# Performance work log

Hardware: AMD Instinct MI355X
Metric: run time of the kernel (lower is better)

The kernel has to match this reference:

```python
import jax, jax.numpy as jnp
import numpy as np

B, T, C, NH, HS, NL, VOCAB = 4, 1024, 768, 12, 64, 6, 128
PRIMES = [2, 3, 5, 7, 11, 13, 17, 19, 23, 29]
NEG_INF = jnp.finfo(jnp.float32).min


def _build_lut(t):
    # lut[n, i] = v_{p_i}(n), p-adic valuation of position n
    lut = np.zeros((t + 1, len(PRIMES)), np.float32)
    for pi, p in enumerate(PRIMES):
        nn = np.arange(t + 1, dtype=np.int64)
        nn[0] = 1  # v_p(0) treated as 0
        while (nn % p == 0).any():
            d = nn % p == 0
            lut[d, pi] += 1.0
            nn[d] //= p
    return lut


def _build_buffers(t):
    lut = _build_lut(t)
    vl = lut[1 : t + 1]  # positions 1..T, [T, 10]
    res = np.minimum(vl[:, None, :], vl[None, :, :]).sum(-1)  # [T, T]
    causal = np.tril(np.ones((t, t), dtype=bool))
    allowed = ((res > 0) | np.eye(t, dtype=bool)) & causal
    rbias = (np.log1p(res) * allowed).astype(np.float32)
    return vl.astype(np.float32), rbias, allowed


def setup_inputs() -> dict:
    key = jax.random.key(0)
    ks = jax.random.split(key, 16)
    s = 0.02
    vl, rbias, allowed = _build_buffers(T)
    return {
        "idx": jax.random.randint(ks[0], (B, T), 0, VOCAB, dtype=jnp.int32),
        "tok_emb": jax.random.normal(ks[1], (VOCAB, C)) * s,
        "pe_w": jax.random.normal(ks[2], (10, C)) * s,
        "pe_b": jnp.zeros((C,)),
        "vlut": jnp.asarray(vl),
        "rbias": jnp.asarray(rbias),
        "allowed": jnp.asarray(allowed),
        "ln1_g": jnp.ones((NL, C)),
        "ln1_b": jnp.zeros((NL, C)),
        "qw": jax.random.normal(ks[3], (NL, NH, C, HS)) * s,
        "kw": jax.random.normal(ks[4], (NL, NH, C, HS)) * s,
        "vw": jax.random.normal(ks[5], (NL, NH, C, HS)) * s,
        "proj_w": jax.random.normal(ks[6], (NL, C, C)) * s,
        "proj_b": jnp.zeros((NL, C)),
        "ln2_g": jnp.ones((NL, C)),
        "ln2_b": jnp.zeros((NL, C)),
        "ff1_w": jax.random.normal(ks[7], (NL, C, 4 * C)) * s,
        "ff1_b": jnp.zeros((NL, 4 * C)),
        "ff2_w": jax.random.normal(ks[8], (NL, 4 * C, C)) * s,
        "ff2_b": jnp.zeros((NL, C)),
        "lnf_g": jnp.ones((C,)),
        "lnf_b": jnp.zeros((C,)),
        "head_w": jax.random.normal(ks[9], (C, VOCAB)) * s,
        "head_b": jnp.zeros((VOCAB,)),
    }


def _ln(x, g, b, eps=1e-5):
    m = x.mean(-1, keepdims=True)
    v = ((x - m) ** 2).mean(-1, keepdims=True)
    return (x - m) * jax.lax.rsqrt(v + eps) * g + b


def reference(idx, tok_emb, pe_w, pe_b, vlut, rbias, allowed,
              ln1_g, ln1_b, qw, kw, vw, proj_w, proj_b,
              ln2_g, ln2_b, ff1_w, ff1_b, ff2_w, ff2_b,
              lnf_g, lnf_b, head_w, head_b):
    # token embedding + spectral positional encoding
    x = tok_emb[idx] + (vlut @ pe_w + pe_b)  # [B, T, C]
    scale = C ** (-0.5)  # NOTE: source scales by full embed dim, not head_size
    for l in range(NL):
        h = _ln(x, ln1_g[l], ln1_b[l])
        q = jnp.einsum("btc,hcd->bhtd", h, qw[l])
        k = jnp.einsum("btc,hcd->bhtd", h, kw[l])
        v = jnp.einsum("btc,hcd->bhtd", h, vw[l])
        w = jnp.einsum("bhtd,bhsd->bhts", q, k) * scale + rbias  # [B,H,T,T]
        w = jnp.where(allowed, w, NEG_INF)
        a = jax.nn.softmax(w, axis=-1)
        o = jnp.einsum("bhts,bhsd->bhtd", a, v)
        o = o.transpose(0, 2, 1, 3).reshape(x.shape[0], x.shape[1], C)
        x = x + o @ proj_w[l] + proj_b[l]
        h2 = _ln(x, ln2_g[l], ln2_b[l])
        x = x + jax.nn.gelu(h2 @ ff1_w[l] + ff1_b[l], approximate=False) @ ff2_w[l] + ff2_b[l]
    return _ln(x, lnf_g, lnf_b) @ head_w + head_b  # [B, T, VOCAB]
```

## Files before the change

kernel.cpp:

```cpp
#include <hip/hip_runtime.h>
#include <hip/hip_bf16.h>
#include <math.h>


#define Bz 4
#define Tz 1024
#define Cz 768
#define NHz 12
#define HSz 64
#define NLz 6
#define VOCABz 128
#define NTOK (Bz * Tz)

typedef __hip_bfloat16 bf16;
typedef __attribute__((ext_vector_type(8))) __bf16 bf16x8;
typedef __attribute__((ext_vector_type(4))) float f32x4;

#define MFMA16(a, b, c) __builtin_amdgcn_mfma_f32_16x16x32_bf16(a, b, c, 0, 0, 0)

__device__ __forceinline__ float bf2f(bf16 x) { return __bfloat162float(x); }
__device__ __forceinline__ bf16 f2bf(float x) { return __float2bfloat16(x); }
__device__ __forceinline__ float ldx(const void* p, size_t i, int f) {
  return f ? bf2f(((const bf16*)p)[i]) : ((const float*)p)[i];
}
__device__ __forceinline__ void async16(const bf16* g, bf16* l) {
  __builtin_amdgcn_global_load_lds(
      (const __attribute__((address_space(1))) unsigned int*)g,
      (__attribute__((address_space(3))) unsigned int*)l, 16, 0, 0);
}

__global__ void detect_kernel(const void* g1, int* flag) {
  if (threadIdx.x == 0) {
    const unsigned short* p = (const unsigned short*)g1;
    int cnt = 0;
    for (int i = 0; i < 64; i++) cnt += (p[i] == 0x3F80u) ? 1 : 0;
    *flag = (cnt >= 60) ? 1 : 0;
  }
}

#define NCONV 15
struct CPack {
  const void* s[NCONV];
  bf16* d[NCONV];
  int n[NCONV];
};
__global__ __launch_bounds__(256) void convert_all(CPack p, const int* __restrict__ flagp) {
  int f = *flagp;
  int stride = gridDim.x * 256;
#pragma unroll 1
  for (int t = 0; t < NCONV; t++) {
    int n = p.n[t];
    const void* src = p.s[t];
    bf16* dst = p.d[t];
    for (int i = blockIdx.x * 256 + threadIdx.x; i < n; i += stride)
      dst[i] = f ? ((const bf16*)src)[i] : f2bf(((const float*)src)[i]);
  }
}

__global__ __launch_bounds__(256) void transpose_tiled(
    const void* __restrict__ src, bf16* __restrict__ dst, int R, int C,
    size_t s_mat, size_t d_base, size_t d_l, size_t d_h, int hmod,
    const int* __restrict__ flagp) {
  __shared__ bf16 t[64][65];
  int f = *flagp;
  int c0 = blockIdx.x * 64, r0 = blockIdx.y * 64;
  int z = blockIdx.z;
  size_t so = (size_t)z * s_mat;
  size_t dofs = d_base + (size_t)(z / hmod) * d_l + (size_t)(z % hmod) * d_h;
  int tr = threadIdx.x >> 2;
  int tc = (threadIdx.x & 3) * 16;
  size_t sbase = so + (size_t)(r0 + tr) * C + c0 + tc;
#pragma unroll
  for (int u = 0; u < 16; u++) t[tr][tc + u] = f2bf(ldx(src, sbase + u, f));
  __syncthreads();
  int wc = threadIdx.x >> 2;
  int wr = (threadIdx.x & 3) * 16;
  bf16* dp = dst + dofs + (size_t)(c0 + wc) * R + r0 + wr;
#pragma unroll
  for (int u = 0; u < 16; u++) dp[u] = t[wr + u][wc];
}

__global__ __launch_bounds__(256) void embed_kernel(
    const int* __restrict__ idx, const bf16* __restrict__ tok_emb,
    const bf16* __restrict__ pe_w, const bf16* __restrict__ pe_b,
    const bf16* __restrict__ vlut, float* __restrict__ x_res) {
  int row = blockIdx.x;
  int t = row % Tz;
  int tok = idx[row];
  float vl[10];
#pragma unroll
  for (int p = 0; p < 10; p++) vl[p] = bf2f(vlut[t * 10 + p]);
  for (int c = threadIdx.x; c < Cz; c += 256) {
    float acc = bf2f(tok_emb[(size_t)tok * Cz + c]) + bf2f(pe_b[c]);
#pragma unroll
    for (int p = 0; p < 10; p++) acc += vl[p] * bf2f(pe_w[p * Cz + c]);
    x_res[(size_t)row * Cz + c] = acc;
  }
}

__global__ __launch_bounds__(256) void ln_kernel(
    const float* __restrict__ x, const bf16* __restrict__ g,
    const bf16* __restrict__ b, bf16* __restrict__ out) {
  __shared__ float r1[4], r2[4];
  int row = blockIdx.x, tid = threadIdx.x;
  const float* xr = x + (size_t)row * Cz;
  float v0 = xr[tid], v1 = xr[tid + 256], v2 = xr[tid + 512];
  float s1 = v0 + v1 + v2, s2 = v0 * v0 + v1 * v1 + v2 * v2;
#pragma unroll
  for (int off = 32; off > 0; off >>= 1) {
    s1 += __shfl_down(s1, off);
    s2 += __shfl_down(s2, off);
  }
  int lane = tid & 63, wid = tid >> 6;
  if (lane == 0) { r1[wid] = s1; r2[wid] = s2; }
  __syncthreads();
  s1 = r1[0] + r1[1] + r1[2] + r1[3];
  s2 = r2[0] + r2[1] + r2[2] + r2[3];
  float m = s1 * (1.0f / Cz);
  float var = s2 * (1.0f / Cz) - m * m;
  float inv = rsqrtf(var + 1e-5f);
  bf16* orow = out + (size_t)row * Cz;
  orow[tid] = f2bf((v0 - m) * inv * bf2f(g[tid]) + bf2f(b[tid]));
  orow[tid + 256] = f2bf((v1 - m) * inv * bf2f(g[tid + 256]) + bf2f(b[tid + 256]));
  orow[tid + 512] = f2bf((v2 - m) * inv * bf2f(g[tid + 512]) + bf2f(b[tid + 512]));
}

template <int MT>
__global__ __launch_bounds__(256) void gemm_mfma(
    const bf16* __restrict__ A, const bf16* __restrict__ Wt,
    const bf16* __restrict__ bias, float* __restrict__ resid,
    void* __restrict__ out, int M, int N, int K, int mode,
    const int* __restrict__ flagp) {
  constexpr int TM = MT * 32;
  constexpr int API = MT / 2;
  __shared__ bf16 ldsA[2][TM * 32];
  __shared__ bf16 ldsB[2][4096];
  int tid = threadIdx.x;
  int lane = tid & 63, w = tid >> 6;
  int wm = (w >> 1) * (MT * 16), wn = (w & 1) * 64;
  int q = lane >> 4, ln = lane & 15;
  int m0 = blockIdx.y * TM, n0 = blockIdx.x * 128;

  const bf16* gA[API];
  const bf16* gB[2];
#pragma unroll
  for (int p = 0; p < API; p++) {
    int o = w * (API * 1024) + p * 1024 + lane * 16;
    int rp = o >> 7, pp = (o >> 4) & 7;
    int pl = pp ^ (rp & 7);
    int row = rp * 2 + (pl >> 2);
    int cb = pl & 3;
    gA[p] = A + (size_t)(m0 + row) * K + cb * 8;
  }
#pragma unroll
  for (int p = 0; p < 2; p++) {
    int o = w * 2048 + p * 1024 + lane * 16;
    int rp = o >> 7, pp = (o >> 4) & 7;
    int pl = pp ^ (rp & 7);
    int row = rp * 2 + (pl >> 2);
    int cb = pl & 3;
    gB[p] = Wt + (size_t)(n0 + row) * K + cb * 8;
  }
  int ppf = (((ln & 1) << 2) | q) ^ (ln >> 1);
  int aoff = wm * 32 + (ln >> 1) * 64 + ppf * 8;
  int boff = wn * 32 + (ln >> 1) * 64 + ppf * 8;

  f32x4 acc[MT][4] = {};
#pragma unroll
  for (int p = 0; p < API; p++)
    async16(gA[p], &ldsA[0][w * (API * 512) + p * 512]);
#pragma unroll
  for (int p = 0; p < 2; p++)
    async16(gB[p], &ldsB[0][w * 1024 + p * 512]);
  int cur = 0;
  for (int k0 = 0; k0 < K; k0 += 32) {
    __syncthreads();
    if (k0 + 32 < K) {
      int nxt = cur ^ 1;
#pragma unroll
      for (int p = 0; p < API; p++)
        async16(gA[p] + k0 + 32, &ldsA[nxt][w * (API * 512) + p * 512]);
#pragma unroll
      for (int p = 0; p < 2; p++)
        async16(gB[p] + k0 + 32, &ldsB[nxt][w * 1024 + p * 512]);
    }
    bf16x8 af[MT], bfr[4];
#pragma unroll
    for (int i = 0; i < MT; i++)
      af[i] = *(const bf16x8*)&ldsA[cur][aoff + i * 512];
#pragma unroll
    for (int j = 0; j < 4; j++)
      bfr[j] = *(const bf16x8*)&ldsB[cur][boff + j * 512];
#pragma unroll
    for (int i = 0; i < MT; i++)
#pragma unroll
      for (int j = 0; j < 4; j++)
        acc[i][j] = MFMA16(af[i], bfr[j], acc[i][j]);
    cur ^= 1;
  }
  int f = *flagp;
  float bj[4];
#pragma unroll
  for (int j = 0; j < 4; j++)
    bj[j] = bias ? bf2f(bias[n0 + wn + j * 16 + ln]) : 0.0f;
#pragma unroll
  for (int i = 0; i < MT; i++) {
#pragma unroll
    for (int j = 0; j < 4; j++) {
      int col = n0 + wn + j * 16 + ln;
#pragma unroll
      for (int r = 0; r < 4; r++) {
        int row = m0 + wm + i * 16 + q * 4 + r;
        float v = acc[i][j][r] + bj[j];
        size_t oi = (size_t)row * N + col;
        if (mode == 0) {
          ((bf16*)out)[oi] = f2bf(v);
        } else if (mode == 1) {
          ((bf16*)out)[oi] = f2bf(v * 0.5f * (1.0f + erff(v * 0.70710678118f)));
        } else if (mode == 2) {
          resid[oi] += v;
        } else {
          if (f) ((bf16*)out)[oi] = f2bf(v);
          else ((float*)out)[oi] = v;
        }
      }
    }
  }
}

#define ATS 72
__global__ __launch_bounds__(256) void transpose_v(
    const bf16* __restrict__ qkv, bf16* __restrict__ Vt) {
  __shared__ bf16 tile[64][ATS];
  int tid = threadIdx.x;
  int s0 = blockIdx.x * 64, bh = blockIdx.y;
  int b = bh / NHz, h = bh % NHz;
  int row = tid >> 2, c0 = (tid & 3) * 16;
  const bf16* src = qkv + ((size_t)(b * Tz + s0 + row)) * (3 * Cz) + 2 * Cz + h * HSz + c0;
  *(uint4*)&tile[row][c0] = *(const uint4*)src;
  *(uint4*)&tile[row][c0 + 8] = *(const uint4*)(src + 8);
  __syncthreads();
  int d = tid >> 2, sc0 = (tid & 3) * 16;
  unsigned int u[8];
#pragma unroll
  for (int m = 0; m < 8; m++) {
    unsigned int lo = *(const unsigned short*)&tile[sc0 + 2 * m][d];
    unsigned int hi = *(const unsigned short*)&tile[sc0 + 2 * m + 1][d];
    u[m] = lo | (hi << 16);
  }
  bf16* dst = Vt + ((size_t)bh * HSz + d) * Tz + s0 + sc0;
  ((uint4*)dst)[0] = make_uint4(u[0], u[1], u[2], u[3]);
  ((uint4*)dst)[1] = make_uint4(u[4], u[5], u[6], u[7]);
}

__global__ __launch_bounds__(256) void attn_flash(
    const bf16* __restrict__ qkv, const bf16* __restrict__ Vt,
    const bf16* __restrict__ rbias, bf16* __restrict__ attn_out) {
  __shared__ bf16 Qs[128][ATS];
  __shared__ bf16 Ks[64][ATS];
  __shared__ bf16 Vs[64][ATS];
  __shared__ bf16 Ps[4][32][ATS];
  int tid = threadIdx.x;
  int lane = tid & 63, w = tid >> 6;
  int q = lane >> 4, ln = lane & 15;
  int qt = 7 - blockIdx.x;
  int t0 = qt * 128, bh = blockIdx.y;
  int b = bh / NHz, h = bh % NHz;
  const float scale = 0.03608439182435161f;
  int srow = tid >> 2, sc = (tid & 3) * 16;
#pragma unroll
  for (int pass = 0; pass < 2; pass++) {
    int r = srow + pass * 64;
    const bf16* src = qkv + ((size_t)(b * Tz + t0 + r)) * (3 * Cz) + h * HSz + sc;
    *(uint4*)&Qs[r][sc] = *(const uint4*)src;
    *(uint4*)&Qs[r][sc + 8] = *(const uint4*)(src + 8);
  }
  float mrow[2][4], lrow[2][4];
  f32x4 Oacc[2][4] = {};
#pragma unroll
  for (int i = 0; i < 2; i++)
#pragma unroll
    for (int r = 0; r < 4; r++) { mrow[i][r] = -3.0e38f; lrow[i][r] = 0.0f; }
  int nk = 2 * qt + 2;

  for (int kt = 0; kt < nk; kt++) {
    int s0 = kt * 64;
    __syncthreads();
    {
      const bf16* ksrc = qkv + ((size_t)(b * Tz + s0 + srow)) * (3 * Cz) + Cz + h * HSz + sc;
      *(uint4*)&Ks[srow][sc] = *(const uint4*)ksrc;
      *(uint4*)&Ks[srow][sc + 8] = *(const uint4*)(ksrc + 8);
      const bf16* vsrc = Vt + ((size_t)bh * HSz + srow) * Tz + s0 + sc;
      *(uint4*)&Vs[srow][sc] = *(const uint4*)vsrc;
      *(uint4*)&Vs[srow][sc + 8] = *(const uint4*)(vsrc + 8);
    }
    __syncthreads();
    f32x4 sacc[2][4] = {};
#pragma unroll
    for (int ks = 0; ks < 64; ks += 32) {
      bf16x8 aq[2];
#pragma unroll
      for (int i = 0; i < 2; i++)
        aq[i] = *(const bf16x8*)&Qs[w * 32 + i * 16 + ln][ks + q * 8];
#pragma unroll
      for (int j = 0; j < 4; j++) {
        bf16x8 bk = *(const bf16x8*)&Ks[j * 16 + ln][ks + q * 8];
#pragma unroll
        for (int i = 0; i < 2; i++) sacc[i][j] = MFMA16(aq[i], bk, sacc[i][j]);
      }
    }
    float sval[2][4][4];
#pragma unroll
    for (int i = 0; i < 2; i++) {
#pragma unroll
      for (int j = 0; j < 4; j++) {
        int s_col = s0 + j * 16 + ln;
#pragma unroll
        for (int r = 0; r < 4; r++) {
          int t_row = t0 + w * 32 + i * 16 + q * 4 + r;
          float rb = bf2f(rbias[(size_t)t_row * Tz + s_col]);
          float v = sacc[i][j][r] * scale + rb;
          bool ok = (s_col <= t_row) && ((rb > 0.0f) || (s_col == t_row));
          sval[i][j][r] = ok ? v : -3.0e38f;
        }
      }
    }
    float pf[2][4][4];
#pragma unroll
    for (int i = 0; i < 2; i++) {
      float rmax[4], psum[4];
#pragma unroll
      for (int r = 0; r < 4; r++)
        rmax[r] = fmaxf(fmaxf(sval[i][0][r], sval[i][1][r]),
                        fmaxf(sval[i][2][r], sval[i][3][r]));
#pragma unroll
      for (int msk = 8; msk >= 1; msk >>= 1)
#pragma unroll
        for (int r = 0; r < 4; r++)
          rmax[r] = fmaxf(rmax[r], __shfl_xor(rmax[r], msk));
      float nme[4], alpha[4];
#pragma unroll
      for (int r = 0; r < 4; r++) {
        float nm = fmaxf(mrow[i][r], rmax[r]);
        nme[r] = (nm < -1.0e37f) ? 0.0f : nm;
        alpha[r] = (mrow[i][r] < -1.0e37f) ? 0.0f : __expf(mrow[i][r] - nm);
        mrow[i][r] = nm;
        psum[r] = 0.0f;
      }
#pragma unroll
      for (int j = 0; j < 4; j++)
#pragma unroll
        for (int r = 0; r < 4; r++) {
          float p = __expf(sval[i][j][r] - nme[r]);
          pf[i][j][r] = p;
          psum[r] += p;
        }
#pragma unroll
      for (int msk = 8; msk >= 1; msk >>= 1)
#pragma unroll
        for (int r = 0; r < 4; r++) psum[r] += __shfl_xor(psum[r], msk);
#pragma unroll
      for (int r = 0; r < 4; r++) lrow[i][r] = alpha[r] * lrow[i][r] + psum[r];
#pragma unroll
      for (int jd = 0; jd < 4; jd++)
#pragma unroll
        for (int r = 0; r < 4; r++) Oacc[i][jd][r] *= alpha[r];
#pragma unroll
      for (int j = 0; j < 4; j++)
#pragma unroll
        for (int r = 0; r < 4; r++)
          Ps[w][i * 16 + q * 4 + r][j * 16 + ln] = f2bf(pf[i][j][r]);
    }
#pragma unroll
    for (int ks = 0; ks < 64; ks += 32) {
      bf16x8 pa[2];
#pragma unroll
      for (int i = 0; i < 2; i++)
        pa[i] = *(const bf16x8*)&Ps[w][i * 16 + ln][ks + q * 8];
#pragma unroll
      for (int jd = 0; jd < 4; jd++) {
        bf16x8 vb = *(const bf16x8*)&Vs[jd * 16 + ln][ks + q * 8];
#pragma unroll
        for (int i = 0; i < 2; i++) Oacc[i][jd] = MFMA16(pa[i], vb, Oacc[i][jd]);
      }
    }
  }
#pragma unroll
  for (int i = 0; i < 2; i++)
#pragma unroll
    for (int r = 0; r < 4; r++) {
      float inv = 1.0f / lrow[i][r];
      int t_row = t0 + w * 32 + i * 16 + q * 4 + r;
#pragma unroll
      for (int jd = 0; jd < 4; jd++) {
        attn_out[(size_t)(b * Tz + t_row) * Cz + h * HSz + jd * 16 + ln] =
            f2bf(Oacc[i][jd][r] * inv);
      }
    }
}

extern "C" void kernel_launch(void* const* d_in, const int* in_sizes, int n_in,
                              void* d_out, int out_size, void* d_ws, size_t ws_size,
                              hipStream_t stream) {
  const int* idx = (const int*)d_in[0];
  int p0 = 7;
  if (n_in == 23) p0 = 6;
  else if (in_sizes[6] != Tz * Tz) p0 = 6;

  const void* r_tok_emb = d_in[1];
  const void* r_pe_w = d_in[2];
  const void* r_pe_b = d_in[3];
  const void* r_vlut = d_in[4];
  const void* r_rbias = d_in[5];
  const void* r_ln1_g = d_in[p0 + 0];
  const void* r_ln1_b = d_in[p0 + 1];
  const void* r_qw = d_in[p0 + 2];
  const void* r_kw = d_in[p0 + 3];
  const void* r_vw = d_in[p0 + 4];
  const void* r_proj_w = d_in[p0 + 5];
  const void* r_proj_b = d_in[p0 + 6];
  const void* r_ln2_g = d_in[p0 + 7];
  const void* r_ln2_b = d_in[p0 + 8];
  const void* r_ff1_w = d_in[p0 + 9];
  const void* r_ff1_b = d_in[p0 + 10];
  const void* r_ff2_w = d_in[p0 + 11];
  const void* r_ff2_b = d_in[p0 + 12];
  const void* r_lnf_g = d_in[p0 + 13];
  const void* r_lnf_b = d_in[p0 + 14];
  const void* r_head_w = d_in[p0 + 15];
  const void* r_head_b = d_in[p0 + 16];

  char* wsp = (char*)d_ws;
  auto alloc = [&](size_t bytes) {
    char* p = wsp;
    wsp += (bytes + 255) & ~(size_t)255;
    return (void*)p;
  };
  int* flag = (int*)alloc(256);
  float* x_res = (float*)alloc((size_t)NTOK * Cz * 4);
  bf16* h = (bf16*)alloc((size_t)NTOK * Cz * 2);
  bf16* qkv = (bf16*)alloc((size_t)NTOK * 3 * Cz * 2);
  bf16* attn = (bf16*)alloc((size_t)NTOK * Cz * 2);
  bf16* ffm = (bf16*)alloc((size_t)NTOK * 4 * Cz * 2);
  bf16* Vt = (bf16*)alloc((size_t)Bz * NHz * HSz * Tz * 2);
  bf16* wqkv_t = (bf16*)alloc((size_t)NLz * 3 * Cz * Cz * 2);
  bf16* proj_t = (bf16*)alloc((size_t)NLz * Cz * Cz * 2);
  bf16* ff1_t = (bf16*)alloc((size_t)NLz * 4 * Cz * Cz * 2);
  bf16* ff2_t = (bf16*)alloc((size_t)NLz * 4 * Cz * Cz * 2);
  bf16* head_t = (bf16*)alloc((size_t)VOCABz * Cz * 2);
  bf16* tok_emb = (bf16*)alloc((size_t)VOCABz * Cz * 2);
  bf16* pe_w = (bf16*)alloc(10 * Cz * 2);
  bf16* pe_b = (bf16*)alloc(Cz * 2);
  bf16* vlut = (bf16*)alloc(Tz * 10 * 2);
  bf16* rbias = (bf16*)alloc((size_t)Tz * Tz * 2);
  bf16* ln1_g = (bf16*)alloc(NLz * Cz * 2);
  bf16* ln1_b = (bf16*)alloc(NLz * Cz * 2);
  bf16* proj_b = (bf16*)alloc(NLz * Cz * 2);
  bf16* ln2_g = (bf16*)alloc(NLz * Cz * 2);
  bf16* ln2_b = (bf16*)alloc(NLz * Cz * 2);
  bf16* ff1_b = (bf16*)alloc(NLz * 4 * Cz * 2);
  bf16* ff2_b = (bf16*)alloc(NLz * Cz * 2);
  bf16* lnf_g = (bf16*)alloc(Cz * 2);
  bf16* lnf_b = (bf16*)alloc(Cz * 2);
  bf16* head_b = (bf16*)alloc(VOCABz * 2);

  detect_kernel<<<1, 64, 0, stream>>>(r_ln1_g, flag);

  CPack cp;
  const void* csrc[NCONV] = {r_tok_emb, r_pe_w, r_pe_b, r_vlut, r_rbias,
                             r_ln1_g, r_ln1_b, r_proj_b, r_ln2_g, r_ln2_b,
                             r_ff1_b, r_ff2_b, r_lnf_g, r_lnf_b, r_head_b};
  bf16* cdst[NCONV] = {tok_emb, pe_w, pe_b, vlut, rbias,
                       ln1_g, ln1_b, proj_b, ln2_g, ln2_b,
                       ff1_b, ff2_b, lnf_g, lnf_b, head_b};
  int cn[NCONV] = {VOCABz * Cz, 10 * Cz, Cz, Tz * 10, Tz * Tz,
                   NLz * Cz, NLz * Cz, NLz * Cz, NLz * Cz, NLz * Cz,
                   NLz * 4 * Cz, NLz * Cz, Cz, Cz, VOCABz};
  for (int i = 0; i < NCONV; i++) { cp.s[i] = csrc[i]; cp.d[i] = cdst[i]; cp.n[i] = cn[i]; }
  convert_all<<<1024, 256, 0, stream>>>(cp, flag);

  for (int g = 0; g < 3; g++) {
    const void* src = (g == 0) ? r_qw : (g == 1) ? r_kw : r_vw;
    transpose_tiled<<<dim3(1, Cz / 64, NLz * NHz), 256, 0, stream>>>(
        src, wqkv_t, Cz, HSz, (size_t)Cz * HSz,
        (size_t)g * Cz * Cz, (size_t)3 * Cz * Cz, (size_t)HSz * Cz, NHz, flag);
  }
  transpose_tiled<<<dim3(Cz / 64, Cz / 64, NLz), 256, 0, stream>>>(
      r_proj_w, proj_t, Cz, Cz, (size_t)Cz * Cz, 0, (size_t)Cz * Cz, 0, 1, flag);
  transpose_tiled<<<dim3(4 * Cz / 64, Cz / 64, NLz), 256, 0, stream>>>(
      r_ff1_w, ff1_t, Cz, 4 * Cz, (size_t)4 * Cz * Cz, 0, (size_t)4 * Cz * Cz, 0, 1, flag);
  transpose_tiled<<<dim3(Cz / 64, 4 * Cz / 64, NLz), 256, 0, stream>>>(
      r_ff2_w, ff2_t, 4 * Cz, Cz, (size_t)4 * Cz * Cz, 0, (size_t)4 * Cz * Cz, 0, 1, flag);
  transpose_tiled<<<dim3(VOCABz / 64, Cz / 64, 1), 256, 0, stream>>>(
      r_head_w, head_t, Cz, VOCABz, 0, 0, 0, 0, 1, flag);

  embed_kernel<<<NTOK, 256, 0, stream>>>(idx, tok_emb, pe_w, pe_b, vlut, x_res);

  for (int l = 0; l < NLz; l++) {
    ln_kernel<<<NTOK, 256, 0, stream>>>(x_res, ln1_g + l * Cz, ln1_b + l * Cz, h);
    gemm_mfma<4><<<dim3(3 * Cz / 128, NTOK / 128), 256, 0, stream>>>(
        h, wqkv_t + (size_t)l * 3 * Cz * Cz, nullptr, nullptr, qkv,
        NTOK, 3 * Cz, Cz, 0, flag);
    transpose_v<<<dim3(Tz / 64, Bz * NHz), 256, 0, stream>>>(qkv, Vt);
    attn_flash<<<dim3(Tz / 128, Bz * NHz), 256, 0, stream>>>(qkv, Vt, rbias, attn);
    gemm_mfma<2><<<dim3(Cz / 128, NTOK / 64), 256, 0, stream>>>(
        attn, proj_t + (size_t)l * Cz * Cz, proj_b + l * Cz, x_res, nullptr,
        NTOK, Cz, Cz, 2, flag);
    ln_kernel<<<NTOK, 256, 0, stream>>>(x_res, ln2_g + l * Cz, ln2_b + l * Cz, h);
    gemm_mfma<4><<<dim3(4 * Cz / 128, NTOK / 128), 256, 0, stream>>>(
        h, ff1_t + (size_t)l * 4 * Cz * Cz, ff1_b + (size_t)l * 4 * Cz, nullptr,
        ffm, NTOK, 4 * Cz, Cz, 1, flag);
    gemm_mfma<2><<<dim3(Cz / 128, NTOK / 64), 256, 0, stream>>>(
        ffm, ff2_t + (size_t)l * 4 * Cz * Cz, ff2_b + l * Cz, x_res, nullptr,
        NTOK, Cz, 4 * Cz, 2, flag);
  }
  ln_kernel<<<NTOK, 256, 0, stream>>>(x_res, lnf_g, lnf_b, h);
  gemm_mfma<2><<<dim3(VOCABz / 128, NTOK / 64), 256, 0, stream>>>(
      h, head_t, head_b, nullptr, d_out, NTOK, VOCABz, Cz, 3, flag);
}
```

Before: 2.116 ms.

## Use one wave per LayerNorm row and smaller attention query tiles with K/V prefetch

LayerNorm now assigns one wavefront per row, so a block handles four rows and the reduction uses only shuffles, with no shared memory or block barrier. The flash-attention kernel shrinks its query tile from 128 to 64 rows, which doubles the grid to give more blocks and less causal waste per block. It also prefetches the next K/V tile into registers while the current tile is being computed. In exchange, each K/V tile is loaded twice as often across blocks and each wave has less MFMA work to hide latency behind.

```diff
diff --git a/kernel.cpp b/kernel.cpp
--- a/kernel.cpp
+++ b/kernel.cpp
@@ -101,28 +101,31 @@
 __global__ __launch_bounds__(256) void ln_kernel(
     const float* __restrict__ x, const bf16* __restrict__ g,
     const bf16* __restrict__ b, bf16* __restrict__ out) {
-  __shared__ float r1[4], r2[4];
-  int row = blockIdx.x, tid = threadIdx.x;
+  int w = threadIdx.x >> 6, lane = threadIdx.x & 63;
+  int row = blockIdx.x * 4 + w;
   const float* xr = x + (size_t)row * Cz;
-  float v0 = xr[tid], v1 = xr[tid + 256], v2 = xr[tid + 512];
-  float s1 = v0 + v1 + v2, s2 = v0 * v0 + v1 * v1 + v2 * v2;
-#pragma unroll
-  for (int off = 32; off > 0; off >>= 1) {
-    s1 += __shfl_down(s1, off);
-    s2 += __shfl_down(s2, off);
-  }
-  int lane = tid & 63, wid = tid >> 6;
-  if (lane == 0) { r1[wid] = s1; r2[wid] = s2; }
-  __syncthreads();
-  s1 = r1[0] + r1[1] + r1[2] + r1[3];
-  s2 = r2[0] + r2[1] + r2[2] + r2[3];
+  float v[12];
+  float s1 = 0.0f, s2 = 0.0f;
+#pragma unroll
+  for (int i = 0; i < 12; i++) {
+    v[i] = xr[lane + i * 64];
+    s1 += v[i];
+    s2 += v[i] * v[i];
+  }
+#pragma unroll
+  for (int off = 32; off >= 1; off >>= 1) {
+    s1 += __shfl_xor(s1, off);
+    s2 += __shfl_xor(s2, off);
+  }
   float m = s1 * (1.0f / Cz);
   float var = s2 * (1.0f / Cz) - m * m;
   float inv = rsqrtf(var + 1e-5f);
   bf16* orow = out + (size_t)row * Cz;
-  orow[tid] = f2bf((v0 - m) * inv * bf2f(g[tid]) + bf2f(b[tid]));
-  orow[tid + 256] = f2bf((v1 - m) * inv * bf2f(g[tid + 256]) + bf2f(b[tid + 256]));
-  orow[tid + 512] = f2bf((v2 - m) * inv * bf2f(g[tid + 512]) + bf2f(b[tid + 512]));
+#pragma unroll
+  for (int i = 0; i < 12; i++) {
+    int c = lane + i * 64;
+    orow[c] = f2bf((v[i] - m) * inv * bf2f(g[c]) + bf2f(b[c]));
+  }
 }
 
 template <int MT>
@@ -256,147 +259,141 @@
 __global__ __launch_bounds__(256) void attn_flash(
     const bf16* __restrict__ qkv, const bf16* __restrict__ Vt,
     const bf16* __restrict__ rbias, bf16* __restrict__ attn_out) {
-  __shared__ bf16 Qs[128][ATS];
+  __shared__ bf16 Qs[64][ATS];
   __shared__ bf16 Ks[64][ATS];
   __shared__ bf16 Vs[64][ATS];
-  __shared__ bf16 Ps[4][32][ATS];
+  __shared__ bf16 Ps[4][16][ATS];
   int tid = threadIdx.x;
   int lane = tid & 63, w = tid >> 6;
   int q = lane >> 4, ln = lane & 15;
-  int qt = 7 - blockIdx.x;
-  int t0 = qt * 128, bh = blockIdx.y;
+  int qt = (int)gridDim.x - 1 - (int)blockIdx.x;
+  int t0 = qt * 64, bh = blockIdx.y;
   int b = bh / NHz, h = bh % NHz;
   const float scale = 0.03608439182435161f;
   int srow = tid >> 2, sc = (tid & 3) * 16;
-#pragma unroll
-  for (int pass = 0; pass < 2; pass++) {
-    int r = srow + pass * 64;
-    const bf16* src = qkv + ((size_t)(b * Tz + t0 + r)) * (3 * Cz) + h * HSz + sc;
-    *(uint4*)&Qs[r][sc] = *(const uint4*)src;
-    *(uint4*)&Qs[r][sc + 8] = *(const uint4*)(src + 8);
-  }
-  float mrow[2][4], lrow[2][4];
-  f32x4 Oacc[2][4] = {};
-#pragma unroll
-  for (int i = 0; i < 2; i++)
-#pragma unroll
-    for (int r = 0; r < 4; r++) { mrow[i][r] = -3.0e38f; lrow[i][r] = 0.0f; }
-  int nk = 2 * qt + 2;
-
+  {
+    const bf16* src = qkv + ((size_t)(b * Tz + t0 + srow)) * (3 * Cz) + h * HSz + sc;
+    *(uint4*)&Qs[srow][sc] = *(const uint4*)src;
+    *(uint4*)&Qs[srow][sc + 8] = *(const uint4*)(src + 8);
+  }
+  float mrow[4], lrow[4];
+  f32x4 Oacc[4] = {};
+#pragma unroll
+  for (int r = 0; r < 4; r++) { mrow[r] = -3.0e38f; lrow[r] = 0.0f; }
+  int t_base = t0 + w * 16 + q * 4;
+  int nk = qt + 1;
+
+  const bf16* kcol = qkv + (size_t)b * Tz * (3 * Cz) + Cz + h * HSz + sc;
+  const bf16* vrow = Vt + ((size_t)bh * HSz + srow) * Tz + sc;
+  uint4 ka, kb, va, vb2;
+  {
+    const bf16* kp = kcol + (size_t)srow * (3 * Cz);
+    ka = *(const uint4*)kp;
+    kb = *(const uint4*)(kp + 8);
+    va = *(const uint4*)vrow;
+    vb2 = *(const uint4*)(vrow + 8);
+  }
   for (int kt = 0; kt < nk; kt++) {
+    __syncthreads();
+    *(uint4*)&Ks[srow][sc] = ka;
+    *(uint4*)&Ks[srow][sc + 8] = kb;
+    *(uint4*)&Vs[srow][sc] = va;
+    *(uint4*)&Vs[srow][sc + 8] = vb2;
+    __syncthreads();
+    if (kt + 1 < nk) {
+      const bf16* kp = kcol + (size_t)(((kt + 1) * 64) + srow) * (3 * Cz);
+      ka = *(const uint4*)kp;
+      kb = *(const uint4*)(kp + 8);
+      const bf16* vp = vrow + (kt + 1) * 64;
+      va = *(const uint4*)vp;
+      vb2 = *(const uint4*)(vp + 8);
+    }
     int s0 = kt * 64;
-    __syncthreads();
-    {
-      const bf16* ksrc = qkv + ((size_t)(b * Tz + s0 + srow)) * (3 * Cz) + Cz + h * HSz + sc;
-      *(uint4*)&Ks[srow][sc] = *(const uint4*)ksrc;
-      *(uint4*)&Ks[srow][sc + 8] = *(const uint4*)(ksrc + 8);
-      const bf16* vsrc = Vt + ((size_t)bh * HSz + srow) * Tz + s0 + sc;
-      *(uint4*)&Vs[srow][sc] = *(const uint4*)vsrc;
-      *(uint4*)&Vs[srow][sc + 8] = *(const uint4*)(vsrc + 8);
-    }
-    __syncthreads();
-    f32x4 sacc[2][4] = {};
+    f32x4 sacc[4] = {};
 #pragma unroll
     for (int ks = 0; ks < 64; ks += 32) {
-      bf16x8 aq[2];
-#pragma unroll
-      for (int i = 0; i < 2; i++)
-        aq[i] = *(const bf16x8*)&Qs[w * 32 + i * 16 + ln][ks + q * 8];
+      bf16x8 aq = *(const bf16x8*)&Qs[w * 16 + ln][ks + q * 8];
 #pragma unroll
       for (int j = 0; j < 4; j++) {
         bf16x8 bk = *(const bf16x8*)&Ks[j * 16 + ln][ks + q * 8];
-#pragma unroll
-        for (int i = 0; i < 2; i++) sacc[i][j] = MFMA16(aq[i], bk, sacc[i][j]);
+        sacc[j] = MFMA16(aq, bk, sacc[j]);
       }
     }
-    float sval[2][4][4];
-#pragma unroll
-    for (int i = 0; i < 2; i++) {
-#pragma unroll
-      for (int j = 0; j < 4; j++) {
-        int s_col = s0 + j * 16 + ln;
-#pragma unroll
-        for (int r = 0; r < 4; r++) {
-          int t_row = t0 + w * 32 + i * 16 + q * 4 + r;
-          float rb = bf2f(rbias[(size_t)t_row * Tz + s_col]);
-          float v = sacc[i][j][r] * scale + rb;
-          bool ok = (s_col <= t_row) && ((rb > 0.0f) || (s_col == t_row));
-          sval[i][j][r] = ok ? v : -3.0e38f;
-        }
+    float sval[4][4];
+#pragma unroll
+    for (int j = 0; j < 4; j++) {
+      int s_col = s0 + j * 16 + ln;
+#pragma unroll
+      for (int r = 0; r < 4; r++) {
+        int t_row = t_base + r;
+        float rb = bf2f(rbias[(size_t)t_row * Tz + s_col]);
+        float v = sacc[j][r] * scale + rb;
+        bool ok = (s_col <= t_row) && ((rb > 0.0f) || (s_col == t_row));
+        sval[j][r] = ok ? v : -3.0e38f;
       }
     }
-    float pf[2][4][4];
-#pragma unroll
-    for (int i = 0; i < 2; i++) {
-      float rmax[4], psum[4];
+    float rmax[4];
+#pragma unroll
+    for (int r = 0; r < 4; r++)
+      rmax[r] = fmaxf(fmaxf(sval[0][r], sval[1][r]), fmaxf(sval[2][r], sval[3][r]));
+#pragma unroll
+    for (int msk = 8; msk >= 1; msk >>= 1)
 #pragma unroll
       for (int r = 0; r < 4; r++)
-        rmax[r] = fmaxf(fmaxf(sval[i][0][r], sval[i][1][r]),
-                        fmaxf(sval[i][2][r], sval[i][3][r]));
-#pragma unroll
-      for (int msk = 8; msk >= 1; msk >>= 1)
-#pragma unroll
-        for (int r = 0; r < 4; r++)
-          rmax[r] = fmaxf(rmax[r], __shfl_xor(rmax[r], msk));
-      float nme[4], alpha[4];
+        rmax[r] = fmaxf(rmax[r], __shfl_xor(rmax[r], msk));
+    float nme[4], alpha[4];
+#pragma unroll
+    for (int r = 0; r < 4; r++) {
+      float nm = fmaxf(mrow[r], rmax[r]);
+      nme[r] = (nm < -1.0e37f) ? 0.0f : nm;
+      alpha[r] = (mrow[r] < -1.0e37f) ? 0.0f : __expf(mrow[r] - nm);
+      mrow[r] = nm;
+    }
+    float pf[4][4];
+    float psum[4] = {0.f, 0.f, 0.f, 0.f};
+#pragma unroll
+    for (int j = 0; j < 4; j++)
 #pragma unroll
       for (int r = 0; r < 4; r++) {
-        float nm = fmaxf(mrow[i][r], rmax[r]);
-        nme[r] = (nm < -1.0e37f) ? 0.0f : nm;
-        alpha[r] = (mrow[i][r] < -1.0e37f) ? 0.0f : __expf(mrow[i][r] - nm);
-        mrow[i][r] = nm;
-        psum[r] = 0.0f;
+        float p = __expf(sval[j][r] - nme[r]);
+        pf[j][r] = p;
+        psum[r] += p;
       }
 #pragma unroll
-      for (int j = 0; j < 4; j++)
-#pragma unroll
-        for (int r = 0; r < 4; r++) {
-          float p = __expf(sval[i][j][r] - nme[r]);
-          pf[i][j][r] = p;
-          psum[r] += p;
-        }
-#pragma unroll
-      for (int msk = 8; msk >= 1; msk >>= 1)
-#pragma unroll
-        for (int r = 0; r < 4; r++) psum[r] += __shfl_xor(psum[r], msk);
-#pragma unroll
-      for (int r = 0; r < 4; r++) lrow[i][r] = alpha[r] * lrow[i][r] + psum[r];
-#pragma unroll
-      for (int jd = 0; jd < 4; jd++)
-#pragma unroll
-        for (int r = 0; r < 4; r++) Oacc[i][jd][r] *= alpha[r];
-#pragma unroll
-      for (int j = 0; j < 4; j++)
-#pragma unroll
-        for (int r = 0; r < 4; r++)
-          Ps[w][i * 16 + q * 4 + r][j * 16 + ln] = f2bf(pf[i][j][r]);
-    }
+    for (int msk = 8; msk >= 1; msk >>= 1)
+#pragma unroll
+      for (int r = 0; r < 4; r++) psum[r] += __shfl_xor(psum[r], msk);
+#pragma unroll
+    for (int r = 0; r < 4; r++) lrow[r] = alpha[r] * lrow[r] + psum[r];
+#pragma unroll
+    for (int jd = 0; jd < 4; jd++)
+#pragma unroll
+      for (int r = 0; r < 4; r++) Oacc[jd][r] *= alpha[r];
+#pragma unroll
+    for (int j = 0; j < 4; j++)
+#pragma unroll
+      for (int r = 0; r < 4; r++)
+        Ps[w][q * 4 + r][j * 16 + ln] = f2bf(pf[j][r]);
 #pragma unroll
     for (int ks = 0; ks < 64; ks += 32) {
-      bf16x8 pa[2];
-#pragma unroll
-      for (int i = 0; i < 2; i++)
-        pa[i] = *(const bf16x8*)&Ps[w][i * 16 + ln][ks + q * 8];
+      bf16x8 pa = *(const bf16x8*)&Ps[w][ln][ks + q * 8];
 #pragma unroll
       for (int jd = 0; jd < 4; jd++) {
         bf16x8 vb = *(const bf16x8*)&Vs[jd * 16 + ln][ks + q * 8];
-#pragma unroll
-        for (int i = 0; i < 2; i++) Oacc[i][jd] = MFMA16(pa[i], vb, Oacc[i][jd]);
+        Oacc[jd] = MFMA16(pa, vb, Oacc[jd]);
       }
     }
   }
 #pragma unroll
-  for (int i = 0; i < 2; i++)
-#pragma unroll
-    for (int r = 0; r < 4; r++) {
-      float inv = 1.0f / lrow[i][r];
-      int t_row = t0 + w * 32 + i * 16 + q * 4 + r;
-#pragma unroll
-      for (int jd = 0; jd < 4; jd++) {
-        attn_out[(size_t)(b * Tz + t_row) * Cz + h * HSz + jd * 16 + ln] =
-            f2bf(Oacc[i][jd][r] * inv);
-      }
-    }
+  for (int r = 0; r < 4; r++) {
+    float inv = 1.0f / lrow[r];
+    int t_row = t_base + r;
+#pragma unroll
+    for (int jd = 0; jd < 4; jd++) {
+      attn_out[(size_t)(b * Tz + t_row) * Cz + h * HSz + jd * 16 + ln] =
+          f2bf(Oacc[jd][r] * inv);
+    }
+  }
 }
 
 extern "C" void kernel_launch(void* const* d_in, const int* in_sizes, int n_in,
@@ -497,16 +494,16 @@
   embed_kernel<<<NTOK, 256, 0, stream>>>(idx, tok_emb, pe_w, pe_b, vlut, x_res);
 
   for (int l = 0; l < NLz; l++) {
-    ln_kernel<<<NTOK, 256, 0, stream>>>(x_res, ln1_g + l * Cz, ln1_b + l * Cz, h);
+    ln_kernel<<<NTOK / 4, 256, 0, stream>>>(x_res, ln1_g + l * Cz, ln1_b + l * Cz, h);
     gemm_mfma<4><<<dim3(3 * Cz / 128, NTOK / 128), 256, 0, stream>>>(
         h, wqkv_t + (size_t)l * 3 * Cz * Cz, nullptr, nullptr, qkv,
         NTOK, 3 * Cz, Cz, 0, flag);
     transpose_v<<<dim3(Tz / 64, Bz * NHz), 256, 0, stream>>>(qkv, Vt);
-    attn_flash<<<dim3(Tz / 128, Bz * NHz), 256, 0, stream>>>(qkv, Vt, rbias, attn);
+    attn_flash<<<dim3(Tz / 64, Bz * NHz), 256, 0, stream>>>(qkv, Vt, rbias, attn);
     gemm_mfma<2><<<dim3(Cz / 128, NTOK / 64), 256, 0, stream>>>(
         attn, proj_t + (size_t)l * Cz * Cz, proj_b + l * Cz, x_res, nullptr,
         NTOK, Cz, Cz, 2, flag);
-    ln_kernel<<<NTOK, 256, 0, stream>>>(x_res, ln2_g + l * Cz, ln2_b + l * Cz, h);
+    ln_kernel<<<NTOK / 4, 256, 0, stream>>>(x_res, ln2_g + l * Cz, ln2_b + l * Cz, h);
     gemm_mfma<4><<<dim3(4 * Cz / 128, NTOK / 128), 256, 0, stream>>>(
         h, ff1_t + (size_t)l * 4 * Cz * Cz, ff1_b + (size_t)l * 4 * Cz, nullptr,
         ffm, NTOK, 4 * Cz, Cz, 1, flag);
@@ -514,7 +511,7 @@
         ffm, ff2_t + (size_t)l * 4 * Cz * Cz, ff2_b + l * Cz, x_res, nullptr,
         NTOK, Cz, 4 * Cz, 2, flag);
   }
-  ln_kernel<<<NTOK, 256, 0, stream>>>(x_res, lnf_g, lnf_b, h);
+  ln_kernel<<<NTOK / 4, 256, 0, stream>>>(x_res, lnf_g, lnf_b, h);
   gemm_mfma<2><<<dim3(VOCABz / 128, NTOK / 64), 256, 0, stream>>>(
       h, head_t, head_b, nullptr, d_out, NTOK, VOCABz, Cz, 3, flag);
 }
```

After: 1.815 ms. 14.2% less time.
